# Kernel tuning notes

Measured on AMD Instinct MI355X. Metric: run time of the kernel, lower is better.

Reference implementation:

```python
import jax, jax.numpy as jnp
import numpy as np

D_MODEL, D_K, D_V, H = 1024, 64, 64, 16
B, NQ, NK = 4, 1024, 1024
HID = D_MODEL // 2


def _dwg(x, W1, b1, W2, b2):
    # DynamicWeightGenerator: sigmoid(fc2(relu(fc1(x))))
    h = jax.nn.relu(jnp.einsum('bnd,hd->bnh', x, W1) + b1)
    return jax.nn.sigmoid(jnp.einsum('bnh,dh->bnd', h, W2) + b2)


def setup_inputs() -> dict:
    key = jax.random.key(0)
    ks = jax.random.split(key, 32)
    s = 0.02
    inp = {
        'queries': jax.random.normal(ks[0], (B, NQ, D_MODEL), jnp.float32),
        'keys': jax.random.normal(ks[1], (B, NK, D_MODEL), jnp.float32),
        'values': jax.random.normal(ks[2], (B, NK, D_MODEL), jnp.float32),
        'attention_mask': jax.random.randint(ks[3], (B, 1, NQ, NK), 0, 2) > 0,
        'attention_weights': jax.random.uniform(ks[4], (B, H, NQ, NK), jnp.float32),
        'memory': jax.random.normal(ks[5], (B, NK), jnp.float32),
        # projections (torch Linear convention: y = x @ W.T + b)
        'Wq': jax.random.normal(ks[6], (H * D_K, D_MODEL), jnp.float32) * s,
        'bq': jnp.zeros((H * D_K,), jnp.float32),
        'Wk': jax.random.normal(ks[7], (H * D_K, D_MODEL), jnp.float32) * s,
        'bk': jnp.zeros((H * D_K,), jnp.float32),
        'Wv': jax.random.normal(ks[8], (H * D_V, D_MODEL), jnp.float32) * s,
        'bv': jnp.zeros((H * D_V,), jnp.float32),
        'Wo': jax.random.normal(ks[9], (D_MODEL, H * D_V), jnp.float32) * s,
        'bo': jnp.zeros((D_MODEL,), jnp.float32),
        'Wmm': jax.random.normal(ks[10], (H * D_V, 1), jnp.float32) * s,
        'bmm': jnp.zeros((H * D_V,), jnp.float32),
    }
    for i, tag in enumerate(['q', 'k', 'v']):
        k0, k1 = ks[11 + 2 * i], ks[12 + 2 * i]
        inp[f'W1{tag}'] = jax.random.normal(k0, (HID, D_MODEL), jnp.float32) * s
        inp[f'b1{tag}'] = jnp.zeros((HID,), jnp.float32)
        inp[f'W2{tag}'] = jax.random.normal(k1, (D_MODEL, HID), jnp.float32) * s
        inp[f'b2{tag}'] = jnp.zeros((D_MODEL,), jnp.float32)
    return inp


def reference(queries, keys, values, attention_mask, attention_weights, memory,
              Wq, bq, Wk, bk, Wv, bv, Wo, bo, Wmm, bmm,
              W1q, b1q, W2q, b2q, W1k, b1k, W2k, b2k, W1v, b1v, W2v, b2v):
    b_s, nq = queries.shape[:2]
    nk = keys.shape[1]
    # dynamic elementwise gating of inputs
    q_in = queries * _dwg(queries, W1q, b1q, W2q, b2q)
    k_in = keys * _dwg(keys, W1k, b1k, W2k, b2k)
    v_in = values * _dwg(values, W1v, b1v, W2v, b2v)
    # projections -> (b, h, n, d)
    q = (jnp.einsum('bnd,ed->bne', q_in, Wq) + bq).reshape(b_s, nq, H, D_K).transpose(0, 2, 1, 3)
    k = (jnp.einsum('bnd,ed->bne', k_in, Wk) + bk).reshape(b_s, nk, H, D_K).transpose(0, 2, 1, 3)
    v = (jnp.einsum('bnd,ed->bne', v_in, Wv) + bv).reshape(b_s, nk, H, D_V).transpose(0, 2, 1, 3)
    # per-token memory factor: fc_mm(memory[..., None]) -> (b, h, nk, d_k)
    mm = (memory[..., None] * Wmm[:, 0] + bmm).reshape(b_s, nk, H, D_K).transpose(0, 2, 1, 3)
    att = jnp.einsum('bhqd,bhkd->bhqk', q, k * mm) / np.sqrt(D_K).astype(np.float32)
    att = att * attention_weights                         # custom scaling (slice [:nk] == full)
    att = jnp.where(attention_mask, -jnp.inf, att)        # masked_fill
    att = jax.nn.softmax(att, axis=-1)
    out = jnp.einsum('bhqk,bhkd->bhqd', att, v * mm)      # (b, h, nq, d_v)
    out = out.transpose(0, 2, 1, 3).reshape(b_s, nq, H * D_V)
    return jnp.einsum('bne,de->bnd', out, Wo) + bo
```

## Files before the change

### kernel.cpp

```cpp
#include <hip/hip_runtime.h>
#include <hip/hip_bf16.h>

#define BB    4
#define NN    1024
#define DM    1024
#define HH    16
#define HID   512
#define TT    (BB * NN)

typedef __attribute__((ext_vector_type(8))) short bf16x8;
typedef __attribute__((ext_vector_type(4))) float f32x4;

__device__ __forceinline__ ushort f2bfu(float f) {
    __hip_bfloat16 h = __float2bfloat16(f);
    return __builtin_bit_cast(ushort, h);
}

__device__ __forceinline__ float bfu2f(ushort u) {
    __hip_bfloat16 h = __builtin_bit_cast(__hip_bfloat16, u);
    return __bfloat162float(h);
}

__device__ __forceinline__ f32x4 mfma16(bf16x8 a, bf16x8 b, f32x4 c) {
    return __builtin_amdgcn_mfma_f32_16x16x32_bf16(a, b, c, 0, 0, 0);
}

__device__ __forceinline__ void gll16(const void* g, void* l) {
    __builtin_amdgcn_global_load_lds(
        (const __attribute__((address_space(1))) unsigned int*)g,
        (__attribute__((address_space(3))) unsigned int*)l, 16, 0, 0);
}

__global__ void detect_mask_kernel(const unsigned char* __restrict__ m,
                                   int nbytes, int* __restrict__ flags) {
    int stride = blockDim.x * gridDim.x;
    int hi = 0, lo = 0;
    for (int i = blockIdx.x * blockDim.x + threadIdx.x; i < nbytes; i += stride) {
        unsigned char v = m[i];
        if (v) { if (i & 3) hi = 1; else lo = 1; }
    }
    if (hi) atomicOr(&flags[0], 1);
    if (lo) atomicOr(&flags[1], 1);
}

template <int NS>
struct CvtArgs { const float* s[NS]; ushort* d[NS]; };

template <int NS>
__global__ __launch_bounds__(256) void cvt_multi(CvtArgs<NS> a, int n4) {
    int total = n4 * NS;
    int stride = blockDim.x * gridDim.x;
    for (int i = blockIdx.x * blockDim.x + threadIdx.x; i < total; i += stride) {
        const float* sp = a.s[0];
        ushort* dp = a.d[0];
        #pragma unroll
        for (int k = 1; k < NS; ++k) {
            bool ge = i >= k * n4;
            sp = ge ? a.s[k] : sp;
            dp = ge ? a.d[k] : dp;
        }
        int j = i % n4;
        float4 v = ((const float4*)sp)[j];
        uint2 o;
        o.x = (unsigned)f2bfu(v.x) | ((unsigned)f2bfu(v.y) << 16);
        o.y = (unsigned)f2bfu(v.z) | ((unsigned)f2bfu(v.w) << 16);
        ((uint2*)dp)[j] = o;
    }
}

struct GB {
    const ushort* A[3]; const ushort* W[3];
    const float* bias[3]; void* C[3]; const ushort* X[3];
};

template <int EP>
__global__ __launch_bounds__(256) void gemm_bf16(
    GB gb, int M, int N, int K,
    const float* __restrict__ mem, const float* __restrict__ Wmm,
    const float* __restrict__ bmm)
{
    __shared__ __align__(16) ushort As[128 * 64];
    __shared__ __align__(16) ushort Bs[128 * 64];
    const int z = blockIdx.z;
    const ushort* A = gb.A[z];
    const ushort* W = gb.W[z];
    const float* bias = gb.bias[z];
    void* Cout = gb.C[z];
    const ushort* X = gb.X[z];

    const int tid = threadIdx.x;
    const int lane = tid & 63, w = tid >> 6;
    const int lc = lane & 15, lg = lane >> 4;
    const int m0 = blockIdx.x * 128, n0 = blockIdx.y * 128;
    const int wm = (w >> 1) * 64, wn = (w & 1) * 64;
    const int srow = lane >> 3, scol = 8 * ((lane & 7) ^ srow);
    const int swl = (lc & 7) << 3;

    f32x4 acc[4][4];
    #pragma unroll
    for (int i = 0; i < 4; ++i)
        #pragma unroll
        for (int j = 0; j < 4; ++j)
            acc[i][j] = (f32x4){0.f, 0.f, 0.f, 0.f};

    #pragma unroll
    for (int ci = 0; ci < 4; ++ci) {
        int c = w + ci * 4;
        gll16(&A[(size_t)(m0 + c * 8 + srow) * K + 0 + scol], &As[c * 512]);
        gll16(&W[(size_t)(n0 + c * 8 + srow) * K + 0 + scol], &Bs[c * 512]);
    }

    for (int k0 = 0; k0 < K; k0 += 64) {
        __syncthreads();
        bf16x8 af[4][2], bfr[4][2];
        #pragma unroll
        for (int mi = 0; mi < 4; ++mi) {
            int row = wm + mi * 16 + lc;
            af[mi][0] = *(const bf16x8*)&As[row * 64 + ((lg * 8) ^ swl)];
            af[mi][1] = *(const bf16x8*)&As[row * 64 + ((32 + lg * 8) ^ swl)];
        }
        #pragma unroll
        for (int nj = 0; nj < 4; ++nj) {
            int row = wn + nj * 16 + lc;
            bfr[nj][0] = *(const bf16x8*)&Bs[row * 64 + ((lg * 8) ^ swl)];
            bfr[nj][1] = *(const bf16x8*)&Bs[row * 64 + ((32 + lg * 8) ^ swl)];
        }
        #pragma unroll
        for (int mi = 0; mi < 4; ++mi)
            #pragma unroll
            for (int nj = 0; nj < 4; ++nj) {
                acc[mi][nj] = mfma16(af[mi][0], bfr[nj][0], acc[mi][nj]);
                acc[mi][nj] = mfma16(af[mi][1], bfr[nj][1], acc[mi][nj]);
            }
        __syncthreads();
        if (k0 + 64 < K) {
            int kn = k0 + 64;
            #pragma unroll
            for (int ci = 0; ci < 4; ++ci) {
                int c = w + ci * 4;
                gll16(&A[(size_t)(m0 + c * 8 + srow) * K + kn + scol], &As[c * 512]);
                gll16(&W[(size_t)(n0 + c * 8 + srow) * K + kn + scol], &Bs[c * 512]);
            }
        }
    }

    #pragma unroll
    for (int nj = 0; nj < 4; ++nj) {
        int e = n0 + wn + nj * 16 + lc;
        float bv = bias[e];
        float wmv = 0.f, bmv = 0.f;
        if (EP == 7) { wmv = Wmm[e]; bmv = bmm[e]; }
        #pragma unroll
        for (int mi = 0; mi < 4; ++mi) {
            int mbase = m0 + wm + mi * 16 + lg * 4;
            if (EP == 7 && z == 2) {
                ushort u[4];
                #pragma unroll
                for (int r = 0; r < 4; ++r) {
                    float v = (acc[mi][nj][r] + bv) * (mem[mbase + r] * wmv + bmv);
                    u[r] = f2bfu(v);
                }
                int bb = mbase >> 10, n = mbase & 1023;
                size_t off = ((size_t)(bb * HH + (e >> 6)) * 64 + (e & 63)) * NN + n;
                uint2 pk;
                pk.x = (unsigned)u[0] | ((unsigned)u[1] << 16);
                pk.y = (unsigned)u[2] | ((unsigned)u[3] << 16);
                *(uint2*)&((ushort*)Cout)[off] = pk;
            } else {
                #pragma unroll
                for (int r = 0; r < 4; ++r) {
                    int m = mbase + r;
                    float v = acc[mi][nj][r] + bv;
                    if (EP == 1) v = fmaxf(v, 0.f);
                    if (EP == 2) v = bfu2f(X[(size_t)m * N + e]) * (1.f / (1.f + __expf(-v)));
                    if (EP == 7) {
                        if (z == 0) v = v * 0.125f;
                        else        v = v * (mem[m] * wmv + bmv);
                    }
                    size_t off = (size_t)m * N + e;
                    if (EP == 4) ((float*)Cout)[off] = v;
                    else         ((ushort*)Cout)[off] = f2bfu(v);
                }
            }
        }
    }
}

__global__ __launch_bounds__(256) void attn_mfma(
    const ushort* __restrict__ qp, const ushort* __restrict__ kp,
    const ushort* __restrict__ vt, const float* __restrict__ aw,
    const void* __restrict__ maskp, const int* __restrict__ mflags,
    ushort* __restrict__ ob)
{
    __shared__ __align__(16) ushort Ks[2][64 * 64];
    __shared__ __align__(16) ushort Vs[2][64 * 64];
    __shared__ __align__(16) ushort Ps[64 * 64];
    const int tid = threadIdx.x, lane = tid & 63, w = tid >> 6;
    const int lc = lane & 15, lg = lane >> 4;
    const int qt = blockIdx.x, bh = blockIdx.y;
    const int b = bh >> 4, h = bh & 15;
    const int q0 = qt * 64, wq = w * 16;
    const int mode = mflags[0] ? (mflags[1] ? 1 : 2) : 0;
    const int srow = lane >> 3, scol = 8 * ((lane & 7) ^ srow);
    const int swl = (lc & 7) << 3;

    const ushort* qrow = &qp[(size_t)(b * NN + q0 + wq + lc) * DM + h * 64];
    bf16x8 bq0 = *(const bf16x8*)&qrow[lg * 8];
    bf16x8 bq1 = *(const bf16x8*)&qrow[32 + lg * 8];

    #pragma unroll
    for (int ci = 0; ci < 2; ++ci) {
        int c = w + ci * 4;
        gll16(&kp[(size_t)(b * NN + c * 8 + srow) * DM + h * 64 + scol], &Ks[0][c * 512]);
        gll16(&vt[(size_t)(bh * 64 + c * 8 + srow) * NN + 0 + scol], &Vs[0][c * 512]);
    }
    __syncthreads();

    f32x4 oacc[4];
    #pragma unroll
    for (int i = 0; i < 4; ++i) oacc[i] = (f32x4){0.f, 0.f, 0.f, 0.f};
    float psum = 0.f;
    const int q = q0 + wq + lc;
    const float* awrow = aw + ((size_t)bh * NN + q) * NN;
    const size_t mrowo = ((size_t)b * NN + q) * NN;

    for (int t = 0; t < 16; ++t) {
        const int k0 = t * 64;
        const int cur = t & 1;
        const ushort* Kc = Ks[cur];
        const ushort* Vc = Vs[cur];

        float4 awv[4];
        #pragma unroll
        for (int mi = 0; mi < 4; ++mi)
            awv[mi] = *(const float4*)&awrow[k0 + mi * 16 + lg * 4];
        int4 mvi[4]; unsigned mvb[4]; float4 mvf[4];
        if (mode == 0) {
            #pragma unroll
            for (int mi = 0; mi < 4; ++mi)
                mvi[mi] = *(const int4*)&((const int*)maskp)[mrowo + k0 + mi * 16 + lg * 4];
        } else if (mode == 1) {
            #pragma unroll
            for (int mi = 0; mi < 4; ++mi)
                mvb[mi] = *(const unsigned*)&((const unsigned char*)maskp)[mrowo + k0 + mi * 16 + lg * 4];
        } else {
            #pragma unroll
            for (int mi = 0; mi < 4; ++mi)
                mvf[mi] = *(const float4*)&((const float*)maskp)[mrowo + k0 + mi * 16 + lg * 4];
        }
        __builtin_amdgcn_sched_barrier(0);

        if (t < 15) {
            int kn = k0 + 64;
            #pragma unroll
            for (int ci = 0; ci < 2; ++ci) {
                int c = w + ci * 4;
                gll16(&kp[(size_t)(b * NN + kn + c * 8 + srow) * DM + h * 64 + scol], &Ks[cur ^ 1][c * 512]);
                gll16(&vt[(size_t)(bh * 64 + c * 8 + srow) * NN + kn + scol], &Vs[cur ^ 1][c * 512]);
            }
        }

        f32x4 sacc[4];
        #pragma unroll
        for (int mi = 0; mi < 4; ++mi) {
            int krow = mi * 16 + lc;
            bf16x8 a0 = *(const bf16x8*)&Kc[krow * 64 + ((lg * 8) ^ swl)];
            bf16x8 a1 = *(const bf16x8*)&Kc[krow * 64 + ((32 + lg * 8) ^ swl)];
            f32x4 s = (f32x4){0.f, 0.f, 0.f, 0.f};
            s = mfma16(a0, bq0, s);
            s = mfma16(a1, bq1, s);
            sacc[mi] = s;
        }

        #pragma unroll
        for (int mi = 0; mi < 4; ++mi) {
            unsigned mk[4];
            if (mode == 0) {
                mk[0] = mvi[mi].x != 0; mk[1] = mvi[mi].y != 0;
                mk[2] = mvi[mi].z != 0; mk[3] = mvi[mi].w != 0;
            } else if (mode == 1) {
                mk[0] = mvb[mi] & 0xffu;        mk[1] = (mvb[mi] >> 8) & 0xffu;
                mk[2] = (mvb[mi] >> 16) & 0xffu; mk[3] = (mvb[mi] >> 24) & 0xffu;
            } else {
                mk[0] = mvf[mi].x != 0.f; mk[1] = mvf[mi].y != 0.f;
                mk[2] = mvf[mi].z != 0.f; mk[3] = mvf[mi].w != 0.f;
            }
            const float aww[4] = {awv[mi].x, awv[mi].y, awv[mi].z, awv[mi].w};
            float pv[4];
            #pragma unroll
            for (int r = 0; r < 4; ++r) {
                float sv = sacc[mi][r] * aww[r];
                pv[r] = mk[r] ? 0.f : __expf(sv);
                psum += pv[r];
            }
            uint2 pk;
            pk.x = (unsigned)f2bfu(pv[0]) | ((unsigned)f2bfu(pv[1]) << 16);
            pk.y = (unsigned)f2bfu(pv[2]) | ((unsigned)f2bfu(pv[3]) << 16);
            *(uint2*)&Ps[(wq + lc) * 64 + ((mi * 16 + lg * 4) ^ swl)] = pk;
        }

        #pragma unroll
        for (int kk = 0; kk < 2; ++kk) {
            bf16x8 pa = *(const bf16x8*)&Ps[(wq + lc) * 64 + ((kk * 32 + lg * 8) ^ swl)];
            #pragma unroll
            for (int nj = 0; nj < 4; ++nj) {
                bf16x8 vb = *(const bf16x8*)&Vc[(nj * 16 + lc) * 64 + ((kk * 32 + lg * 8) ^ swl)];
                oacc[nj] = mfma16(pa, vb, oacc[nj]);
            }
        }
        __syncthreads();
    }

    psum += __shfl_xor(psum, 16);
    psum += __shfl_xor(psum, 32);
    float inv = 1.0f / psum;
    float invr[4];
    #pragma unroll
    for (int r = 0; r < 4; ++r)
        invr[r] = __shfl(inv, (lane & 48) | (lg * 4 + r));

    #pragma unroll
    for (int nj = 0; nj < 4; ++nj)
        #pragma unroll
        for (int r = 0; r < 4; ++r) {
            int qq = q0 + wq + lg * 4 + r;
            float v = oacc[nj][r] * invr[r];
            ob[(size_t)(b * NN + qq) * DM + h * 64 + nj * 16 + lc] = f2bfu(v);
        }
}

extern "C" void kernel_launch(void* const* d_in, const int* in_sizes, int n_in,
                              void* d_out, int out_size, void* d_ws, size_t ws_size,
                              hipStream_t stream) {
    const float* xin_f[3] = {(const float*)d_in[0], (const float*)d_in[1], (const float*)d_in[2]};
    const void*  maskp   = d_in[3];
    const float* aw      = (const float*)d_in[4];
    const float* memv    = (const float*)d_in[5];
    const float* Wp_f[3] = {(const float*)d_in[6], (const float*)d_in[8], (const float*)d_in[10]};
    const float* bp[3]   = {(const float*)d_in[7], (const float*)d_in[9], (const float*)d_in[11]};
    const float* Wo_f  = (const float*)d_in[12];  const float* bo  = (const float*)d_in[13];
    const float* Wmm = (const float*)d_in[14];    const float* bmm = (const float*)d_in[15];
    const float* W1f[3] = {(const float*)d_in[16], (const float*)d_in[20], (const float*)d_in[24]};
    const float* b1a[3] = {(const float*)d_in[17], (const float*)d_in[21], (const float*)d_in[25]};
    const float* W2f[3] = {(const float*)d_in[18], (const float*)d_in[22], (const float*)d_in[26]};
    const float* b2a[3] = {(const float*)d_in[19], (const float*)d_in[23], (const float*)d_in[27]};

    char* p = (char*)d_ws;
    auto alloc = [&](size_t bytes) { char* r = p; p += (bytes + 255) & ~(size_t)255; return r; };
    int*    mflags = (int*)alloc(256);
    ushort* xbf[3]; for (int t = 0; t < 3; ++t) xbf[t] = (ushort*)alloc((size_t)TT * DM * 2);
    ushort* Wpb[3]; for (int t = 0; t < 3; ++t) Wpb[t] = (ushort*)alloc((size_t)DM * DM * 2);
    ushort* Wob  = (ushort*)alloc((size_t)DM * DM * 2);
    ushort* W1b[3]; for (int t = 0; t < 3; ++t) W1b[t] = (ushort*)alloc((size_t)HID * DM * 2);
    ushort* W2b[3]; for (int t = 0; t < 3; ++t) W2b[t] = (ushort*)alloc((size_t)DM * HID * 2);
    ushort* hbuf[3]; for (int t = 0; t < 3; ++t) hbuf[t] = (ushort*)alloc((size_t)TT * HID * 2);
    ushort* xg[3];  for (int t = 0; t < 3; ++t) xg[t] = (ushort*)alloc((size_t)TT * DM * 2);
    ushort* qpb  = (ushort*)alloc((size_t)TT * DM * 2);
    ushort* ksb  = (ushort*)alloc((size_t)TT * DM * 2);
    ushort* vtb  = (ushort*)alloc((size_t)TT * DM * 2);
    ushort* obuf = (ushort*)alloc((size_t)TT * DM * 2);

    hipMemsetAsync(mflags, 0, 8, stream);
    detect_mask_kernel<<<512, 256, 0, stream>>>((const unsigned char*)maskp,
                                                BB * NN * NN, mflags);

    {
        CvtArgs<3> a;
        for (int t = 0; t < 3; ++t) { a.s[t] = xin_f[t]; a.d[t] = xbf[t]; }
        cvt_multi<3><<<2048, 256, 0, stream>>>(a, TT * DM / 4);
    }
    {
        CvtArgs<4> a;
        a.s[0] = Wp_f[0]; a.d[0] = Wpb[0];
        a.s[1] = Wp_f[1]; a.d[1] = Wpb[1];
        a.s[2] = Wp_f[2]; a.d[2] = Wpb[2];
        a.s[3] = Wo_f;    a.d[3] = Wob;
        cvt_multi<4><<<2048, 256, 0, stream>>>(a, DM * DM / 4);
    }
    {
        CvtArgs<6> a;
        for (int t = 0; t < 3; ++t) { a.s[t] = W1f[t]; a.d[t] = W1b[t]; }
        for (int t = 0; t < 3; ++t) { a.s[3 + t] = W2f[t]; a.d[3 + t] = W2b[t]; }
        cvt_multi<6><<<2048, 256, 0, stream>>>(a, HID * DM / 4);
    }

    const dim3 blk(256);
    GB g1 = {}, g2 = {}, g3 = {}, g4 = {};
    for (int t = 0; t < 3; ++t) {
        g1.A[t] = xbf[t];  g1.W[t] = W1b[t]; g1.bias[t] = b1a[t]; g1.C[t] = hbuf[t];
        g2.A[t] = hbuf[t]; g2.W[t] = W2b[t]; g2.bias[t] = b2a[t]; g2.C[t] = xg[t]; g2.X[t] = xbf[t];
        g3.A[t] = xg[t];   g3.W[t] = Wpb[t]; g3.bias[t] = bp[t];
    }
    g3.C[0] = qpb; g3.C[1] = ksb; g3.C[2] = vtb;
    g4.A[0] = obuf; g4.W[0] = Wob; g4.bias[0] = bo; g4.C[0] = d_out;

    gemm_bf16<1><<<dim3(TT / 128, HID / 128, 3), blk, 0, stream>>>(g1, TT, HID, DM, nullptr, nullptr, nullptr);
    gemm_bf16<2><<<dim3(TT / 128, DM / 128, 3), blk, 0, stream>>>(g2, TT, DM, HID, nullptr, nullptr, nullptr);
    gemm_bf16<7><<<dim3(TT / 128, DM / 128, 3), blk, 0, stream>>>(g3, TT, DM, DM, memv, Wmm, bmm);

    attn_mfma<<<dim3(NN / 64, BB * HH), blk, 0, stream>>>(qpb, ksb, vtb, aw,
                                                          maskp, mflags, obuf);

    gemm_bf16<4><<<dim3(TT / 128, DM / 128, 1), blk, 0, stream>>>(g4, TT, DM, DM, nullptr, nullptr, nullptr);
}
```

Before: 316.3 us.

## Double-buffer GEMM tiles, narrow N tiles, drop LDS staging in attention, vectorize mask scan

The GEMM now double-buffers its A/B tiles in LDS with explicit vmcnt waits, so global loads for tile t+2 overlap compute on tile t. It also gains a template for a narrower N tile (64 columns) used on the smaller GEMMs to launch more blocks. The attention kernel stops staging K and V through LDS and reads them directly from global memory into MFMA operands, removing barriers but relying on cache for reuse across waves. The mask detection kernel reads 16 bytes per load instead of one byte.

```diff
diff --git a/kernel.cpp b/kernel.cpp
--- a/kernel.cpp
+++ b/kernel.cpp
@@ -31,13 +31,15 @@
         (__attribute__((address_space(3))) unsigned int*)l, 16, 0, 0);
 }
 
-__global__ void detect_mask_kernel(const unsigned char* __restrict__ m,
-                                   int nbytes, int* __restrict__ flags) {
+__global__ void detect_mask_kernel(const uint4* __restrict__ m,
+                                   int n16, int* __restrict__ flags) {
     int stride = blockDim.x * gridDim.x;
-    int hi = 0, lo = 0;
-    for (int i = blockIdx.x * blockDim.x + threadIdx.x; i < nbytes; i += stride) {
-        unsigned char v = m[i];
-        if (v) { if (i & 3) hi = 1; else lo = 1; }
+    unsigned hi = 0, lo = 0;
+    for (int i = blockIdx.x * blockDim.x + threadIdx.x; i < n16; i += stride) {
+        uint4 v = m[i];
+        unsigned o = v.x | v.y | v.z | v.w;
+        lo |= o & 0xFFu;
+        hi |= o & 0xFFFFFF00u;
     }
     if (hi) atomicOr(&flags[0], 1);
     if (lo) atomicOr(&flags[1], 1);
@@ -73,14 +75,14 @@
     const float* bias[3]; void* C[3]; const ushort* X[3];
 };
 
-template <int EP>
+template <int EP, int NF>
 __global__ __launch_bounds__(256) void gemm_bf16(
     GB gb, int M, int N, int K,
     const float* __restrict__ mem, const float* __restrict__ Wmm,
     const float* __restrict__ bmm)
 {
-    __shared__ __align__(16) ushort As[128 * 64];
-    __shared__ __align__(16) ushort Bs[128 * 64];
+    __shared__ __align__(16) ushort As[2][128 * 64];
+    __shared__ __align__(16) ushort Bs[2][NF * 32 * 64];
     const int z = blockIdx.z;
     const ushort* A = gb.A[z];
     const ushort* W = gb.W[z];
@@ -91,61 +93,73 @@
     const int tid = threadIdx.x;
     const int lane = tid & 63, w = tid >> 6;
     const int lc = lane & 15, lg = lane >> 4;
-    const int m0 = blockIdx.x * 128, n0 = blockIdx.y * 128;
-    const int wm = (w >> 1) * 64, wn = (w & 1) * 64;
+    const int m0 = blockIdx.x * 128, n0 = blockIdx.y * (NF * 32);
+    const int wm = (w >> 1) * 64, wn = (w & 1) * (NF * 16);
     const int srow = lane >> 3, scol = 8 * ((lane & 7) ^ srow);
     const int swl = (lc & 7) << 3;
 
-    f32x4 acc[4][4];
+    f32x4 acc[4][NF];
     #pragma unroll
     for (int i = 0; i < 4; ++i)
         #pragma unroll
-        for (int j = 0; j < 4; ++j)
+        for (int j = 0; j < NF; ++j)
             acc[i][j] = (f32x4){0.f, 0.f, 0.f, 0.f};
 
-    #pragma unroll
-    for (int ci = 0; ci < 4; ++ci) {
-        int c = w + ci * 4;
-        gll16(&A[(size_t)(m0 + c * 8 + srow) * K + 0 + scol], &As[c * 512]);
-        gll16(&W[(size_t)(n0 + c * 8 + srow) * K + 0 + scol], &Bs[c * 512]);
-    }
-
-    for (int k0 = 0; k0 < K; k0 += 64) {
-        __syncthreads();
-        bf16x8 af[4][2], bfr[4][2];
+    auto stage = [&](int buf, int k0) {
+        #pragma unroll
+        for (int ci = 0; ci < 4; ++ci) {
+            int c = w + ci * 4;
+            gll16(&A[(size_t)(m0 + c * 8 + srow) * K + k0 + scol], &As[buf][c * 512]);
+            if (c < NF * 4)
+                gll16(&W[(size_t)(n0 + c * 8 + srow) * K + k0 + scol], &Bs[buf][c * 512]);
+        }
+    };
+
+    stage(0, 0);
+    stage(1, 64);
+    const int nt = K / 64;
+
+    for (int t = 0; t < nt; ++t) {
+        const int cur = t & 1;
+        if (t < nt - 1) {
+            if constexpr (NF == 4) asm volatile("s_waitcnt vmcnt(8)" ::: "memory");
+            else                   asm volatile("s_waitcnt vmcnt(6)" ::: "memory");
+        } else {
+            asm volatile("s_waitcnt vmcnt(0)" ::: "memory");
+        }
+        __builtin_amdgcn_sched_barrier(0);
+        __builtin_amdgcn_s_barrier();
+
+        bf16x8 af[4][2], bfr[NF][2];
         #pragma unroll
         for (int mi = 0; mi < 4; ++mi) {
             int row = wm + mi * 16 + lc;
-            af[mi][0] = *(const bf16x8*)&As[row * 64 + ((lg * 8) ^ swl)];
-            af[mi][1] = *(const bf16x8*)&As[row * 64 + ((32 + lg * 8) ^ swl)];
-        }
-        #pragma unroll
-        for (int nj = 0; nj < 4; ++nj) {
+            af[mi][0] = *(const bf16x8*)&As[cur][row * 64 + ((lg * 8) ^ swl)];
+            af[mi][1] = *(const bf16x8*)&As[cur][row * 64 + ((32 + lg * 8) ^ swl)];
+        }
+        #pragma unroll
+        for (int nj = 0; nj < NF; ++nj) {
             int row = wn + nj * 16 + lc;
-            bfr[nj][0] = *(const bf16x8*)&Bs[row * 64 + ((lg * 8) ^ swl)];
-            bfr[nj][1] = *(const bf16x8*)&Bs[row * 64 + ((32 + lg * 8) ^ swl)];
-        }
+            bfr[nj][0] = *(const bf16x8*)&Bs[cur][row * 64 + ((lg * 8) ^ swl)];
+            bfr[nj][1] = *(const bf16x8*)&Bs[cur][row * 64 + ((32 + lg * 8) ^ swl)];
+        }
+        asm volatile("s_waitcnt lgkmcnt(0)" ::: "memory");
+        __builtin_amdgcn_sched_barrier(0);
+        __builtin_amdgcn_s_barrier();
+
+        if (t + 2 < nt) stage(cur, (t + 2) * 64);
+
         #pragma unroll
         for (int mi = 0; mi < 4; ++mi)
             #pragma unroll
-            for (int nj = 0; nj < 4; ++nj) {
+            for (int nj = 0; nj < NF; ++nj) {
                 acc[mi][nj] = mfma16(af[mi][0], bfr[nj][0], acc[mi][nj]);
                 acc[mi][nj] = mfma16(af[mi][1], bfr[nj][1], acc[mi][nj]);
             }
-        __syncthreads();
-        if (k0 + 64 < K) {
-            int kn = k0 + 64;
-            #pragma unroll
-            for (int ci = 0; ci < 4; ++ci) {
-                int c = w + ci * 4;
-                gll16(&A[(size_t)(m0 + c * 8 + srow) * K + kn + scol], &As[c * 512]);
-                gll16(&W[(size_t)(n0 + c * 8 + srow) * K + kn + scol], &Bs[c * 512]);
-            }
-        }
-    }
-
-    #pragma unroll
-    for (int nj = 0; nj < 4; ++nj) {
+    }
+
+    #pragma unroll
+    for (int nj = 0; nj < NF; ++nj) {
         int e = n0 + wn + nj * 16 + lc;
         float bv = bias[e];
         float wmv = 0.f, bmv = 0.f;
@@ -192,8 +206,6 @@
     const void* __restrict__ maskp, const int* __restrict__ mflags,
     ushort* __restrict__ ob)
 {
-    __shared__ __align__(16) ushort Ks[2][64 * 64];
-    __shared__ __align__(16) ushort Vs[2][64 * 64];
     __shared__ __align__(16) ushort Ps[64 * 64];
     const int tid = threadIdx.x, lane = tid & 63, w = tid >> 6;
     const int lc = lane & 15, lg = lane >> 4;
@@ -201,20 +213,11 @@
     const int b = bh >> 4, h = bh & 15;
     const int q0 = qt * 64, wq = w * 16;
     const int mode = mflags[0] ? (mflags[1] ? 1 : 2) : 0;
-    const int srow = lane >> 3, scol = 8 * ((lane & 7) ^ srow);
     const int swl = (lc & 7) << 3;
 
     const ushort* qrow = &qp[(size_t)(b * NN + q0 + wq + lc) * DM + h * 64];
     bf16x8 bq0 = *(const bf16x8*)&qrow[lg * 8];
     bf16x8 bq1 = *(const bf16x8*)&qrow[32 + lg * 8];
-
-    #pragma unroll
-    for (int ci = 0; ci < 2; ++ci) {
-        int c = w + ci * 4;
-        gll16(&kp[(size_t)(b * NN + c * 8 + srow) * DM + h * 64 + scol], &Ks[0][c * 512]);
-        gll16(&vt[(size_t)(bh * 64 + c * 8 + srow) * NN + 0 + scol], &Vs[0][c * 512]);
-    }
-    __syncthreads();
 
     f32x4 oacc[4];
     #pragma unroll
@@ -226,9 +229,6 @@
 
     for (int t = 0; t < 16; ++t) {
         const int k0 = t * 64;
-        const int cur = t & 1;
-        const ushort* Kc = Ks[cur];
-        const ushort* Vc = Vs[cur];
 
         float4 awv[4];
         #pragma unroll
@@ -248,24 +248,13 @@
             for (int mi = 0; mi < 4; ++mi)
                 mvf[mi] = *(const float4*)&((const float*)maskp)[mrowo + k0 + mi * 16 + lg * 4];
         }
-        __builtin_amdgcn_sched_barrier(0);
-
-        if (t < 15) {
-            int kn = k0 + 64;
-            #pragma unroll
-            for (int ci = 0; ci < 2; ++ci) {
-                int c = w + ci * 4;
-                gll16(&kp[(size_t)(b * NN + kn + c * 8 + srow) * DM + h * 64 + scol], &Ks[cur ^ 1][c * 512]);
-                gll16(&vt[(size_t)(bh * 64 + c * 8 + srow) * NN + kn + scol], &Vs[cur ^ 1][c * 512]);
-            }
-        }
 
         f32x4 sacc[4];
         #pragma unroll
         for (int mi = 0; mi < 4; ++mi) {
-            int krow = mi * 16 + lc;
-            bf16x8 a0 = *(const bf16x8*)&Kc[krow * 64 + ((lg * 8) ^ swl)];
-            bf16x8 a1 = *(const bf16x8*)&Kc[krow * 64 + ((32 + lg * 8) ^ swl)];
+            const ushort* krow = &kp[(size_t)(b * NN + k0 + mi * 16 + lc) * DM + h * 64];
+            bf16x8 a0 = *(const bf16x8*)&krow[lg * 8];
+            bf16x8 a1 = *(const bf16x8*)&krow[32 + lg * 8];
             f32x4 s = (f32x4){0.f, 0.f, 0.f, 0.f};
             s = mfma16(a0, bq0, s);
             s = mfma16(a1, bq1, s);
@@ -279,7 +268,7 @@
                 mk[0] = mvi[mi].x != 0; mk[1] = mvi[mi].y != 0;
                 mk[2] = mvi[mi].z != 0; mk[3] = mvi[mi].w != 0;
             } else if (mode == 1) {
-                mk[0] = mvb[mi] & 0xffu;        mk[1] = (mvb[mi] >> 8) & 0xffu;
+                mk[0] = mvb[mi] & 0xffu;         mk[1] = (mvb[mi] >> 8) & 0xffu;
                 mk[2] = (mvb[mi] >> 16) & 0xffu; mk[3] = (mvb[mi] >> 24) & 0xffu;
             } else {
                 mk[0] = mvf[mi].x != 0.f; mk[1] = mvf[mi].y != 0.f;
@@ -304,11 +293,10 @@
             bf16x8 pa = *(const bf16x8*)&Ps[(wq + lc) * 64 + ((kk * 32 + lg * 8) ^ swl)];
             #pragma unroll
             for (int nj = 0; nj < 4; ++nj) {
-                bf16x8 vb = *(const bf16x8*)&Vc[(nj * 16 + lc) * 64 + ((kk * 32 + lg * 8) ^ swl)];
+                bf16x8 vb = *(const bf16x8*)&vt[((size_t)bh * 64 + nj * 16 + lc) * NN + k0 + kk * 32 + lg * 8];
                 oacc[nj] = mfma16(pa, vb, oacc[nj]);
             }
         }
-        __syncthreads();
     }
 
     psum += __shfl_xor(psum, 16);
@@ -361,8 +349,8 @@
     ushort* obuf = (ushort*)alloc((size_t)TT * DM * 2);
 
     hipMemsetAsync(mflags, 0, 8, stream);
-    detect_mask_kernel<<<512, 256, 0, stream>>>((const unsigned char*)maskp,
-                                                BB * NN * NN, mflags);
+    detect_mask_kernel<<<256, 256, 0, stream>>>((const uint4*)maskp,
+                                                BB * NN * NN / 16, mflags);
 
     {
         CvtArgs<3> a;
@@ -394,12 +382,12 @@
     g3.C[0] = qpb; g3.C[1] = ksb; g3.C[2] = vtb;
     g4.A[0] = obuf; g4.W[0] = Wob; g4.bias[0] = bo; g4.C[0] = d_out;
 
-    gemm_bf16<1><<<dim3(TT / 128, HID / 128, 3), blk, 0, stream>>>(g1, TT, HID, DM, nullptr, nullptr, nullptr);
-    gemm_bf16<2><<<dim3(TT / 128, DM / 128, 3), blk, 0, stream>>>(g2, TT, DM, HID, nullptr, nullptr, nullptr);
-    gemm_bf16<7><<<dim3(TT / 128, DM / 128, 3), blk, 0, stream>>>(g3, TT, DM, DM, memv, Wmm, bmm);
+    gemm_bf16<1, 2><<<dim3(TT / 128, HID / 64, 3), blk, 0, stream>>>(g1, TT, HID, DM, nullptr, nullptr, nullptr);
+    gemm_bf16<2, 4><<<dim3(TT / 128, DM / 128, 3), blk, 0, stream>>>(g2, TT, DM, HID, nullptr, nullptr, nullptr);
+    gemm_bf16<7, 4><<<dim3(TT / 128, DM / 128, 3), blk, 0, stream>>>(g3, TT, DM, DM, memv, Wmm, bmm);
 
     attn_mfma<<<dim3(NN / 64, BB * HH), blk, 0, stream>>>(qpb, ksb, vtb, aw,
                                                           maskp, mflags, obuf);
 
-    gemm_bf16<4><<<dim3(TT / 128, DM / 128, 1), blk, 0, stream>>>(g4, TT, DM, DM, nullptr, nullptr, nullptr);
-}
+    gemm_bf16<4, 2><<<dim3(TT / 128, DM / 64, 1), blk, 0, stream>>>(g4, TT, DM, DM, nullptr, nullptr, nullptr);
+}
```

Measured after the change: 396.8 us. +25.4%, slower.
